# Kernel tuning notes

Hardware: AMD Instinct MI355X
Metric: run time of the kernel (lower is better)

The kernel has to match this reference:

```python
import jax, jax.numpy as jnp
import numpy as np

# ADMM hyperparameters for mode='only_tv'
GAMMA_TV = 10.0
ALPHA = 5.0
LAMBDA_TV = 1e-4
N_ITERS = 50


def soft_thresh(v, t):
    return jnp.sign(v) * jnp.maximum(jnp.abs(v) - t, 0.0)


def setup_inputs() -> dict:
    key = jax.random.key(0)
    k1, k2, k3 = jax.random.split(key, 3)
    target = jax.random.normal(k1, (4096,), dtype=jnp.float32)
    A = jax.random.normal(k2, (9, 4096), dtype=jnp.float32)  # [M, N], post-transpose
    x0 = jax.random.normal(k3, (4096,), dtype=jnp.float32)   # replaces torch.randn_like
    return {"target": target, "A": A, "x0": x0}


def reference(target, A, x0):
    N = A.shape[1]
    I = jnp.eye(N, dtype=A.dtype)
    Delta = jnp.roll(I, 1, axis=1) - I               # [N, N] circular difference
    DtD = Delta.T @ Delta
    AtA = A.T @ A
    # only_tv: gamma_l1 = beta = 0, so regularizer is ATA + gamma_tv*DtD + alpha*I
    inv_item = jnp.linalg.inv(AtA + GAMMA_TV * DtD + ALPHA * I)

    b = A @ target            # [M]
    bA = b @ A                # [N], constant across iterations

    def step(carry, _):
        x, eta_tv, tau = carry
        # u_tv: soft-threshold of backward difference (roll along axis 0)
        u_tv = soft_thresh(jnp.roll(x, 1, axis=0) - x + eta_tv / GAMMA_TV,
                           LAMBDA_TV / GAMMA_TV)
        # w: nonnegativity split variable
        w = jnp.maximum(x + tau / ALPHA, 0.0)
        # x-update (zero terms for l1/dwt/z dropped: gamma_l1 = gamma_dwt = beta = 0)
        resid = bA + (GAMMA_TV * u_tv - eta_tv) + (ALPHA * w - tau)
        x = resid @ inv_item
        # dual updates
        eta_tv = eta_tv + GAMMA_TV * (Delta @ x - u_tv)
        tau = tau + ALPHA * (x - w)
        return (x, eta_tv, tau), None

    zeros = jnp.zeros_like(x0)
    (x, _, _), _ = jax.lax.scan(step, (x0, zeros, zeros), None, length=N_ITERS)
    return x
```

## Files before the change

### kernel.cpp

```cpp
#include <hip/hip_runtime.h>
#include <math.h>

#define NT 512
#define EPT 8
#define NN 4096
#define MM 9
#define NIT 50

#define W256_1 3.90625e-3f
#define W256_2 1.52587890625e-5f
#define W256_3 5.9604644775390625e-8f
#define K1LAST 0.3333282470703125f

template<int CTRL, int RMASK>
__device__ __forceinline__ float dpp_add(float v) {
  int m = __builtin_amdgcn_update_dpp(0, __builtin_bit_cast(int, v), CTRL, RMASK, 0xf, false);
  return v + __builtin_bit_cast(float, m);
}
__device__ __forceinline__ float wave_sum(float v) {
  v = dpp_add<0x111, 0xf>(v);
  v = dpp_add<0x112, 0xf>(v);
  v = dpp_add<0x114, 0xf>(v);
  v = dpp_add<0x118, 0xf>(v);
  v = dpp_add<0x142, 0xa>(v);
  v = dpp_add<0x143, 0xc>(v);
  return v;
}
template<int CTRL>
__device__ __forceinline__ float dpp_shift(float oldv, float v) {
  int m = __builtin_amdgcn_update_dpp(__builtin_bit_cast(int, oldv),
                                      __builtin_bit_cast(int, v), CTRL, 0xf, 0xf, false);
  return __builtin_bit_cast(float, m);
}

__device__ __forceinline__ void block_reduce9(const float pq[MM], float* __restrict__ s_part,
                                              float* __restrict__ dest, int destStride,
                                              int identCol, int t) {
#pragma unroll
  for (int m = 0; m < MM; ++m) s_part[m * NT + t] = pq[m];
  __syncthreads();
  const int wave = t >> 6, lane = t & 63;
  for (int m = wave; m < MM; m += NT / 64) {
    float s = 0.f;
#pragma unroll
    for (int k = 0; k < NT / 64; ++k) s += s_part[m * NT + lane + 64 * k];
#pragma unroll
    for (int off = 32; off; off >>= 1) s += __shfl_xor(s, off, 64);
    if (lane == 0) dest[m * destStride] = s + ((m == identCol) ? 1.f : 0.f);
  }
  __syncthreads();
}

__device__ __forceinline__ void solveM_pre(const float r[EPT], float pl0[EPT],
                                           float2* __restrict__ s_sc, int t) {
  float yl[EPT];
  yl[EPT - 1] = r[EPT - 1] * 0.1f;
#pragma unroll
  for (int j = EPT - 2; j >= 0; --j) yl[j] = fmaf(0.5f, yl[j + 1], r[j] * 0.1f);
  pl0[0] = 0.5f * yl[0];
#pragma unroll
  for (int j = 1; j < EPT; ++j) pl0[j] = 0.5f * (yl[j] + pl0[j - 1]);
  s_sc[t] = make_float2(yl[0], pl0[EPT - 1]);
}

__device__ __forceinline__ void solveM_post(const float pl0[EPT], float p[EPT],
                                            const float2* __restrict__ s_sc, int t) {
  const float K1[EPT] = {0.001953125f, 0.0048828125f, 0.01025390625f, 0.020751953125f,
                         0.0416259765625f, 0.08331298828125f, 0.166656494140625f,
                         0.3333282470703125f};
  float2 g[9];
#pragma unroll
  for (int k = 0; k < 9; ++k) g[k] = s_sc[(t + k - 4) & (NT - 1)];
  float c = fmaf(W256_3, g[8].x, fmaf(W256_2, g[7].x, fmaf(W256_1, g[6].x, g[5].x)));
  float s1 = fmaf(W256_3, g[0].y, fmaf(W256_2, g[1].y, fmaf(W256_1, g[2].y, g[3].y)));
  float s2 = g[4].x;
  s2 = fmaf(W256_1, g[3].x + g[5].x, s2);
  s2 = fmaf(W256_2, g[2].x + g[6].x, s2);
  s2 = fmaf(W256_3, g[1].x + g[7].x, s2);
  float c2 = fmaf(K1LAST, s2, s1);
  float f2 = 0.5f;
#pragma unroll
  for (int j = 0; j < EPT; ++j) {
    p[j] = fmaf(c2, f2, fmaf(c, K1[j], pl0[j]));
    f2 *= 0.5f;
  }
}

__device__ __forceinline__ void solveM_full(const float r[EPT], float p[EPT],
                                            float2* __restrict__ s_sc, int t) {
  float pl0[EPT];
  solveM_pre(r, pl0, s_sc, t);
  __syncthreads();
  solveM_post(pl0, p, s_sc, t);
}

__global__ void __launch_bounds__(NT, 2)
admm_kernel(const float* __restrict__ tg, const float* __restrict__ Ag,
            const float* __restrict__ x0, float* __restrict__ out) {
  __shared__ float s_part[MM * NT];
  __shared__ float2 s_sc[NT];
  __shared__ float2 s_sc2[NT];
  __shared__ __align__(16) float s_wq[8][12];
  __shared__ float s_q[MM];
  __shared__ float s_S[MM * MM];
  __shared__ float s_Sinv[MM * MM];
  __shared__ float s_L[MM * MM];
  __shared__ float s_edge[8][2];

  const int t = threadIdx.x;
  const int base = t * EPT;
  const int lane = t & 63, wave = t >> 6;

  float A[MM][EPT];
#pragma unroll
  for (int m = 0; m < MM; ++m) {
    float4 a0 = *(const float4*)(Ag + m * NN + base);
    float4 a1 = *(const float4*)(Ag + m * NN + base + 4);
    A[m][0] = a0.x; A[m][1] = a0.y; A[m][2] = a0.z; A[m][3] = a0.w;
    A[m][4] = a1.x; A[m][5] = a1.y; A[m][6] = a1.z; A[m][7] = a1.w;
  }

  float x[EPT], tgt[EPT];
  {
    float4 v0 = *(const float4*)(x0 + base);
    float4 v1 = *(const float4*)(x0 + base + 4);
    x[0] = v0.x; x[1] = v0.y; x[2] = v0.z; x[3] = v0.w;
    x[4] = v1.x; x[5] = v1.y; x[6] = v1.z; x[7] = v1.w;
    float4 t0 = *(const float4*)(tg + base);
    float4 t1 = *(const float4*)(tg + base + 4);
    tgt[0] = t0.x; tgt[1] = t0.y; tgt[2] = t0.z; tgt[3] = t0.w;
    tgt[4] = t1.x; tgt[5] = t1.y; tgt[6] = t1.z; tgt[7] = t1.w;
  }
  if (lane == 0)  s_edge[wave][0] = x[0];
  if (lane == 63) s_edge[wave][1] = x[7];

  float pq[MM];
#pragma unroll
  for (int m = 0; m < MM; ++m) {
    float s = 0.f;
#pragma unroll
    for (int j = 0; j < EPT; ++j) s = fmaf(A[m][j], tgt[j], s);
    pq[m] = s;
  }
  block_reduce9(pq, s_part, s_q, 1, -1, t);

  float bA[EPT];
  {
    float bv[MM];
#pragma unroll
    for (int m = 0; m < MM; ++m) bv[m] = s_q[m];
#pragma unroll
    for (int j = 0; j < EPT; ++j) {
      float s = 0.f;
#pragma unroll
      for (int m = 0; m < MM; ++m) s = fmaf(bv[m], A[m][j], s);
      bA[j] = s;
    }
  }

#pragma unroll
  for (int mcol = 0; mcol < MM; ++mcol) {
    float rin[EPT], gcol[EPT];
#pragma unroll
    for (int j = 0; j < EPT; ++j) rin[j] = A[mcol][j];
    solveM_full(rin, gcol, (mcol & 1) ? s_sc2 : s_sc, t);
#pragma unroll
    for (int k = 0; k < MM; ++k) {
      float s = 0.f;
#pragma unroll
      for (int j = 0; j < EPT; ++j) s = fmaf(A[k][j], gcol[j], s);
      pq[k] = s;
    }
    block_reduce9(pq, s_part, &s_S[mcol], MM, mcol, t);
  }

  if (t < 64) {
    float row[2 * MM];
#pragma unroll
    for (int j = 0; j < MM; ++j) row[j] = (t < MM) ? s_S[t * MM + j] : 0.f;
#pragma unroll
    for (int j = 0; j < MM; ++j) row[MM + j] = (j == t) ? 1.f : 0.f;
#pragma unroll
    for (int pp = 0; pp < MM; ++pp) {
      float pr[2 * MM];
#pragma unroll
      for (int j = 0; j < 2 * MM; ++j) pr[j] = __shfl(row[j], pp, 64);
      float rpiv = 1.f / pr[pp];
      float fct = row[pp] * rpiv;
#pragma unroll
      for (int j = 0; j < 2 * MM; ++j)
        row[j] = (t == pp) ? pr[j] * rpiv : fmaf(-fct, pr[j], row[j]);
    }
    if (t < MM) {
#pragma unroll
      for (int j = 0; j < MM; ++j) s_Sinv[t * MM + j] = row[MM + j];
    }
  }
  __syncthreads();

  if (t < 64) {
    float row[MM];
#pragma unroll
    for (int j = 0; j < MM; ++j) row[j] = (t < MM) ? s_Sinv[t * MM + j] : 0.f;
#pragma unroll
    for (int k = 0; k < MM; ++k) {
      float dk = __shfl(row[k], k, 64);
      float inv = 1.f / sqrtf(dk);
      row[k] *= inv;
#pragma unroll
      for (int jj = k + 1; jj < MM; ++jj) {
        float ljk = __shfl(row[k], jj, 64);
        row[jj] = fmaf(-row[k], ljk, row[jj]);
      }
    }
    if (t < MM) {
#pragma unroll
      for (int j = 0; j < MM; ++j) s_L[t * MM + j] = (t >= j) ? row[j] : 0.f;
    }
  }
  __syncthreads();

  float GH[MM][EPT];
#pragma unroll
  for (int m = 0; m < MM; ++m) {
    float lcol[MM];
#pragma unroll
    for (int k = 0; k < MM; ++k) lcol[k] = s_L[k * MM + m];
    float rhs[EPT];
#pragma unroll
    for (int j = 0; j < EPT; ++j) {
      float s = 0.f;
#pragma unroll
      for (int k = 0; k < MM; ++k) s = fmaf(A[k][j], lcol[k], s);
      rhs[j] = s;
    }
    float gh[EPT];
    solveM_full(rhs, gh, (m & 1) ? s_sc2 : s_sc, t);
#pragma unroll
    for (int j = 0; j < EPT; ++j) GH[m][j] = gh[j];
  }

  float eta[EPT], tau[EPT];
#pragma unroll
  for (int j = 0; j < EPT; ++j) { eta[j] = 0.f; tau[j] = 0.f; }
  float u7prev = 0.f, w7prev = 0.f;

#pragma unroll 1
  for (int it = 0; it < NIT; ++it) {
    float oldm = 0.f, oldn = 0.f;
    if (lane == 0)  oldm = s_edge[(wave + 7) & 7][1];
    if (lane == 63) oldn = s_edge[(wave + 1) & 7][0];
    float xm1 = dpp_shift<0x138>(oldm, x[7]);
    if (it) {
      float xn8 = dpp_shift<0x130>(oldn, x[0]);
      eta[7] = fmaf(10.f, (xn8 - x[7]) - u7prev, eta[7]);
      tau[7] = fmaf(5.f, x[7] - w7prev, tau[7]);
    }
    float u[EPT], w[EPT], r[EPT];
#pragma unroll
    for (int j = 0; j < EPT; ++j) {
      float xprev = (j == 0) ? xm1 : x[j - 1];
      float v = xprev - x[j] + eta[j] * 0.1f;
      float a = fabsf(v) - 1e-5f;
      u[j] = (a > 0.f) ? copysignf(a, v) : 0.f;
      w[j] = fmaxf(fmaf(tau[j], 0.2f, x[j]), 0.f);
      r[j] = bA[j] + 10.f * u[j] - eta[j] + 5.f * w[j] - tau[j];
    }
    float zp[MM];
#pragma unroll
    for (int m = 0; m < MM; ++m) {
      float s = 0.f;
#pragma unroll
      for (int j = 0; j < EPT; ++j) s = fmaf(GH[m][j], r[j], s);
      zp[m] = wave_sum(s);
    }
    if (lane == 63) {
      *(float4*)&s_wq[wave][0] = make_float4(zp[0], zp[1], zp[2], zp[3]);
      *(float4*)&s_wq[wave][4] = make_float4(zp[4], zp[5], zp[6], zp[7]);
      s_wq[wave][8] = zp[8];
    }
    float pl0[EPT];
    solveM_pre(r, pl0, s_sc, t);
    __syncthreads();
    float p[EPT];
    solveM_post(pl0, p, s_sc, t);
    float z[MM];
    {
      float4 a0 = *(const float4*)&s_wq[0][0];
      float4 a1 = *(const float4*)&s_wq[0][4];
      float  a2 = s_wq[0][8];
      z[0] = a0.x; z[1] = a0.y; z[2] = a0.z; z[3] = a0.w;
      z[4] = a1.x; z[5] = a1.y; z[6] = a1.z; z[7] = a1.w; z[8] = a2;
#pragma unroll
      for (int wv = 1; wv < 8; ++wv) {
        float4 b0 = *(const float4*)&s_wq[wv][0];
        float4 b1 = *(const float4*)&s_wq[wv][4];
        float  b2 = s_wq[wv][8];
        z[0] += b0.x; z[1] += b0.y; z[2] += b0.z; z[3] += b0.w;
        z[4] += b1.x; z[5] += b1.y; z[6] += b1.z; z[7] += b1.w; z[8] += b2;
      }
    }
    float xn[EPT];
#pragma unroll
    for (int j = 0; j < EPT; ++j) {
      float s = p[j];
#pragma unroll
      for (int m = 0; m < MM; ++m) s = fmaf(-GH[m][j], z[m], s);
      xn[j] = s;
    }
    if (lane == 0)  s_edge[wave][0] = xn[0];
    if (lane == 63) s_edge[wave][1] = xn[7];
#pragma unroll
    for (int j = 0; j < EPT - 1; ++j) {
      eta[j] = fmaf(10.f, (xn[j + 1] - xn[j]) - u[j], eta[j]);
      tau[j] = fmaf(5.f, xn[j] - w[j], tau[j]);
    }
    u7prev = u[7]; w7prev = w[7];
#pragma unroll
    for (int j = 0; j < EPT; ++j) x[j] = xn[j];
    __syncthreads();
  }

  float4 o0, o1;
  o0.x = x[0]; o0.y = x[1]; o0.z = x[2]; o0.w = x[3];
  o1.x = x[4]; o1.y = x[5]; o1.z = x[6]; o1.w = x[7];
  *(float4*)(out + base) = o0;
  *(float4*)(out + base + 4) = o1;
}

extern "C" void kernel_launch(void* const* d_in, const int* in_sizes, int n_in,
                              void* d_out, int out_size, void* d_ws, size_t ws_size,
                              hipStream_t stream) {
  const float* target = (const float*)d_in[0];
  const float* A      = (const float*)d_in[1];
  const float* x0     = (const float*)d_in[2];
  admm_kernel<<<1, NT, 0, stream>>>(target, A, x0, (float*)d_out);
}
```

Before: 122.6 us.

## Reuse solved columns for GH, use wave-sum reductions, and shorten the stencil

Replaces the shared-memory block reductions in setup with DPP wave sums plus a small per-wave staging array. The solved columns G are kept in registers and GH is formed as a linear combination of them, which removes nine more tridiagonal-type solves and their barriers. The Gauss-Jordan inverse and the Cholesky step are merged into a single pass, dropping one barrier. The solve's neighbour stencil is truncated from 9 to 7 taps. In the main loop, z is reduced by lanes 0-8 and broadcast with readlane instead of every thread summing all waves. The truncated stencil drops weights near 6e-8 and the lane-based reduction changes summation order, so results may differ slightly.

Result: faster. 106.5 us (-13.2%).

```diff
diff --git a/kernel.cpp b/kernel.cpp
--- a/kernel.cpp
+++ b/kernel.cpp
@@ -7,9 +7,8 @@
 #define MM 9
 #define NIT 50
 
-#define W256_1 3.90625e-3f
-#define W256_2 1.52587890625e-5f
-#define W256_3 5.9604644775390625e-8f
+#define LAM  3.90625e-3f
+#define LAM2 1.52587890625e-5f
 #define K1LAST 0.3333282470703125f
 
 template<int CTRL, int RMASK>
@@ -32,23 +31,8 @@
                                       __builtin_bit_cast(int, v), CTRL, 0xf, 0xf, false);
   return __builtin_bit_cast(float, m);
 }
-
-__device__ __forceinline__ void block_reduce9(const float pq[MM], float* __restrict__ s_part,
-                                              float* __restrict__ dest, int destStride,
-                                              int identCol, int t) {
-#pragma unroll
-  for (int m = 0; m < MM; ++m) s_part[m * NT + t] = pq[m];
-  __syncthreads();
-  const int wave = t >> 6, lane = t & 63;
-  for (int m = wave; m < MM; m += NT / 64) {
-    float s = 0.f;
-#pragma unroll
-    for (int k = 0; k < NT / 64; ++k) s += s_part[m * NT + lane + 64 * k];
-#pragma unroll
-    for (int off = 32; off; off >>= 1) s += __shfl_xor(s, off, 64);
-    if (lane == 0) dest[m * destStride] = s + ((m == identCol) ? 1.f : 0.f);
-  }
-  __syncthreads();
+__device__ __forceinline__ float bcast_lane(float v, int l) {
+  return __builtin_bit_cast(float, __builtin_amdgcn_readlane(__builtin_bit_cast(int, v), l));
 }
 
 __device__ __forceinline__ void solveM_pre(const float r[EPT], float pl0[EPT],
@@ -68,15 +52,14 @@
   const float K1[EPT] = {0.001953125f, 0.0048828125f, 0.01025390625f, 0.020751953125f,
                          0.0416259765625f, 0.08331298828125f, 0.166656494140625f,
                          0.3333282470703125f};
-  float2 g[9];
-#pragma unroll
-  for (int k = 0; k < 9; ++k) g[k] = s_sc[(t + k - 4) & (NT - 1)];
-  float c = fmaf(W256_3, g[8].x, fmaf(W256_2, g[7].x, fmaf(W256_1, g[6].x, g[5].x)));
-  float s1 = fmaf(W256_3, g[0].y, fmaf(W256_2, g[1].y, fmaf(W256_1, g[2].y, g[3].y)));
-  float s2 = g[4].x;
-  s2 = fmaf(W256_1, g[3].x + g[5].x, s2);
-  s2 = fmaf(W256_2, g[2].x + g[6].x, s2);
-  s2 = fmaf(W256_3, g[1].x + g[7].x, s2);
+  float2 g[7];
+#pragma unroll
+  for (int k = 0; k < 7; ++k) g[k] = s_sc[(t + k - 3) & (NT - 1)];
+  float c  = fmaf(LAM2, g[6].x, fmaf(LAM, g[5].x, g[4].x));
+  float s1 = fmaf(LAM2, g[0].y, fmaf(LAM, g[1].y, g[2].y));
+  float s2 = g[3].x;
+  s2 = fmaf(LAM, g[2].x + g[4].x, s2);
+  s2 = fmaf(LAM2, g[1].x + g[5].x, s2);
   float c2 = fmaf(K1LAST, s2, s1);
   float f2 = 0.5f;
 #pragma unroll
@@ -86,24 +69,12 @@
   }
 }
 
-__device__ __forceinline__ void solveM_full(const float r[EPT], float p[EPT],
-                                            float2* __restrict__ s_sc, int t) {
-  float pl0[EPT];
-  solveM_pre(r, pl0, s_sc, t);
-  __syncthreads();
-  solveM_post(pl0, p, s_sc, t);
-}
-
 __global__ void __launch_bounds__(NT, 2)
 admm_kernel(const float* __restrict__ tg, const float* __restrict__ Ag,
             const float* __restrict__ x0, float* __restrict__ out) {
-  __shared__ float s_part[MM * NT];
   __shared__ float2 s_sc[NT];
-  __shared__ float2 s_sc2[NT];
   __shared__ __align__(16) float s_wq[8][12];
-  __shared__ float s_q[MM];
   __shared__ float s_S[MM * MM];
-  __shared__ float s_Sinv[MM * MM];
   __shared__ float s_L[MM * MM];
   __shared__ float s_edge[8][2];
 
@@ -140,38 +111,65 @@
     float s = 0.f;
 #pragma unroll
     for (int j = 0; j < EPT; ++j) s = fmaf(A[m][j], tgt[j], s);
-    pq[m] = s;
-  }
-  block_reduce9(pq, s_part, s_q, 1, -1, t);
-
+    pq[m] = wave_sum(s);
+  }
+  if (lane == 63) {
+    *(float4*)&s_wq[wave][0] = make_float4(pq[0], pq[1], pq[2], pq[3]);
+    *(float4*)&s_wq[wave][4] = make_float4(pq[4], pq[5], pq[6], pq[7]);
+    s_wq[wave][8] = pq[8];
+  }
+  __syncthreads();
+  float bb[MM];
+  {
+    float zv = 0.f;
+    if (lane < MM) {
+#pragma unroll
+      for (int wv = 0; wv < 8; ++wv) zv += s_wq[wv][lane];
+    }
+#pragma unroll
+    for (int m = 0; m < MM; ++m) bb[m] = bcast_lane(zv, m);
+  }
   float bA[EPT];
-  {
-    float bv[MM];
-#pragma unroll
-    for (int m = 0; m < MM; ++m) bv[m] = s_q[m];
-#pragma unroll
-    for (int j = 0; j < EPT; ++j) {
-      float s = 0.f;
-#pragma unroll
-      for (int m = 0; m < MM; ++m) s = fmaf(bv[m], A[m][j], s);
-      bA[j] = s;
-    }
-  }
-
-#pragma unroll
-  for (int mcol = 0; mcol < MM; ++mcol) {
-    float rin[EPT], gcol[EPT];
-#pragma unroll
-    for (int j = 0; j < EPT; ++j) rin[j] = A[mcol][j];
-    solveM_full(rin, gcol, (mcol & 1) ? s_sc2 : s_sc, t);
+#pragma unroll
+  for (int j = 0; j < EPT; ++j) {
+    float s = 0.f;
+#pragma unroll
+    for (int m = 0; m < MM; ++m) s = fmaf(bb[m], A[m][j], s);
+    bA[j] = s;
+  }
+
+  float G[MM][EPT];
+#pragma unroll
+  for (int mc = 0; mc < MM; ++mc) {
+    float rin[EPT];
+#pragma unroll
+    for (int j = 0; j < EPT; ++j) rin[j] = A[mc][j];
+    float pl0[EPT];
+    solveM_pre(rin, pl0, s_sc, t);
+    __syncthreads();
+    float gcol[EPT];
+    solveM_post(pl0, gcol, s_sc, t);
+#pragma unroll
+    for (int j = 0; j < EPT; ++j) G[mc][j] = gcol[j];
 #pragma unroll
     for (int k = 0; k < MM; ++k) {
       float s = 0.f;
 #pragma unroll
       for (int j = 0; j < EPT; ++j) s = fmaf(A[k][j], gcol[j], s);
-      pq[k] = s;
-    }
-    block_reduce9(pq, s_part, &s_S[mcol], MM, mcol, t);
+      pq[k] = wave_sum(s);
+    }
+    if (lane == 63) {
+      *(float4*)&s_wq[wave][0] = make_float4(pq[0], pq[1], pq[2], pq[3]);
+      *(float4*)&s_wq[wave][4] = make_float4(pq[4], pq[5], pq[6], pq[7]);
+      s_wq[wave][8] = pq[8];
+    }
+    __syncthreads();
+    if (wave == 0 && lane < MM) {
+      float s = 0.f;
+#pragma unroll
+      for (int wv = 0; wv < 8; ++wv) s += s_wq[wv][lane];
+      s_S[lane * MM + mc] = s + ((lane == mc) ? 1.f : 0.f);
+    }
   }
 
   if (t < 64) {
@@ -191,31 +189,23 @@
       for (int j = 0; j < 2 * MM; ++j)
         row[j] = (t == pp) ? pr[j] * rpiv : fmaf(-fct, pr[j], row[j]);
     }
+    float crow[MM];
+#pragma unroll
+    for (int j = 0; j < MM; ++j) crow[j] = row[MM + j];
+#pragma unroll
+    for (int k = 0; k < MM; ++k) {
+      float dk = __shfl(crow[k], k, 64);
+      float inv = 1.f / sqrtf(dk);
+      crow[k] *= inv;
+#pragma unroll
+      for (int jj = k + 1; jj < MM; ++jj) {
+        float ljk = __shfl(crow[k], jj, 64);
+        crow[jj] = fmaf(-crow[k], ljk, crow[jj]);
+      }
+    }
     if (t < MM) {
 #pragma unroll
-      for (int j = 0; j < MM; ++j) s_Sinv[t * MM + j] = row[MM + j];
-    }
-  }
-  __syncthreads();
-
-  if (t < 64) {
-    float row[MM];
-#pragma unroll
-    for (int j = 0; j < MM; ++j) row[j] = (t < MM) ? s_Sinv[t * MM + j] : 0.f;
-#pragma unroll
-    for (int k = 0; k < MM; ++k) {
-      float dk = __shfl(row[k], k, 64);
-      float inv = 1.f / sqrtf(dk);
-      row[k] *= inv;
-#pragma unroll
-      for (int jj = k + 1; jj < MM; ++jj) {
-        float ljk = __shfl(row[k], jj, 64);
-        row[jj] = fmaf(-row[k], ljk, row[jj]);
-      }
-    }
-    if (t < MM) {
-#pragma unroll
-      for (int j = 0; j < MM; ++j) s_L[t * MM + j] = (t >= j) ? row[j] : 0.f;
+      for (int j = 0; j < MM; ++j) s_L[t * MM + j] = (t >= j) ? crow[j] : 0.f;
     }
   }
   __syncthreads();
@@ -226,18 +216,14 @@
     float lcol[MM];
 #pragma unroll
     for (int k = 0; k < MM; ++k) lcol[k] = s_L[k * MM + m];
-    float rhs[EPT];
 #pragma unroll
     for (int j = 0; j < EPT; ++j) {
       float s = 0.f;
 #pragma unroll
-      for (int k = 0; k < MM; ++k) s = fmaf(A[k][j], lcol[k], s);
-      rhs[j] = s;
-    }
-    float gh[EPT];
-    solveM_full(rhs, gh, (m & 1) ? s_sc2 : s_sc, t);
-#pragma unroll
-    for (int j = 0; j < EPT; ++j) GH[m][j] = gh[j];
+      for (int k = 0; k < MM; ++k)
+        if (k >= m) s = fmaf(G[k][j], lcol[k], s);
+      GH[m][j] = s;
+    }
   }
 
   float eta[EPT], tau[EPT];
@@ -261,8 +247,7 @@
     for (int j = 0; j < EPT; ++j) {
       float xprev = (j == 0) ? xm1 : x[j - 1];
       float v = xprev - x[j] + eta[j] * 0.1f;
-      float a = fabsf(v) - 1e-5f;
-      u[j] = (a > 0.f) ? copysignf(a, v) : 0.f;
+      u[j] = copysignf(fmaxf(fabsf(v) - 1e-5f, 0.f), v);
       w[j] = fmaxf(fmaf(tau[j], 0.2f, x[j]), 0.f);
       r[j] = bA[j] + 10.f * u[j] - eta[j] + 5.f * w[j] - tau[j];
     }
@@ -284,40 +269,29 @@
     __syncthreads();
     float p[EPT];
     solveM_post(pl0, p, s_sc, t);
+    float zv = 0.f;
+    if (lane < MM) {
+#pragma unroll
+      for (int wv = 0; wv < 8; ++wv) zv += s_wq[wv][lane];
+    }
     float z[MM];
-    {
-      float4 a0 = *(const float4*)&s_wq[0][0];
-      float4 a1 = *(const float4*)&s_wq[0][4];
-      float  a2 = s_wq[0][8];
-      z[0] = a0.x; z[1] = a0.y; z[2] = a0.z; z[3] = a0.w;
-      z[4] = a1.x; z[5] = a1.y; z[6] = a1.z; z[7] = a1.w; z[8] = a2;
-#pragma unroll
-      for (int wv = 1; wv < 8; ++wv) {
-        float4 b0 = *(const float4*)&s_wq[wv][0];
-        float4 b1 = *(const float4*)&s_wq[wv][4];
-        float  b2 = s_wq[wv][8];
-        z[0] += b0.x; z[1] += b0.y; z[2] += b0.z; z[3] += b0.w;
-        z[4] += b1.x; z[5] += b1.y; z[6] += b1.z; z[7] += b1.w; z[8] += b2;
-      }
-    }
-    float xn[EPT];
+#pragma unroll
+    for (int m = 0; m < MM; ++m) z[m] = bcast_lane(zv, m);
 #pragma unroll
     for (int j = 0; j < EPT; ++j) {
       float s = p[j];
 #pragma unroll
       for (int m = 0; m < MM; ++m) s = fmaf(-GH[m][j], z[m], s);
-      xn[j] = s;
-    }
-    if (lane == 0)  s_edge[wave][0] = xn[0];
-    if (lane == 63) s_edge[wave][1] = xn[7];
+      x[j] = s;
+    }
+    if (lane == 0)  s_edge[wave][0] = x[0];
+    if (lane == 63) s_edge[wave][1] = x[7];
 #pragma unroll
     for (int j = 0; j < EPT - 1; ++j) {
-      eta[j] = fmaf(10.f, (xn[j + 1] - xn[j]) - u[j], eta[j]);
-      tau[j] = fmaf(5.f, xn[j] - w[j], tau[j]);
+      eta[j] = fmaf(10.f, (x[j + 1] - x[j]) - u[j], eta[j]);
+      tau[j] = fmaf(5.f, x[j] - w[j], tau[j]);
     }
     u7prev = u[7]; w7prev = w[7];
-#pragma unroll
-    for (int j = 0; j < EPT; ++j) x[j] = xn[j];
     __syncthreads();
   }
 
```
